# Performance work log

Hardware: AMD Instinct MI355X
Metric: run time of the kernel (lower is better)

The kernel has to match this reference:

```python
import jax, jax.numpy as jnp
import numpy as np

NEG = -100000.0  # matches torch masked_fill constant

def setup_inputs() -> dict:
    key = jax.random.key(0)
    k1, k2, k3, k4 = jax.random.split(key, 4)
    B, T, D, H, S = 8, 2048, 1024, 8, 128
    features = jax.random.normal(k1, (B, T, D), dtype=jnp.float32)
    begins = jax.random.randint(k2, (B, S), 0, 2016, dtype=jnp.int64)
    widths = jax.random.randint(k3, (B, S), 1, 33, dtype=jnp.int64)
    ends = jnp.minimum(begins + widths, T)
    key_w = jax.random.normal(k4, (H, D), dtype=jnp.float32) / np.sqrt(D)
    key_b = jnp.zeros((H,), dtype=jnp.float32)
    return {"features": features, "begins": begins, "ends": ends,
            "key_w": key_w, "key_b": key_b}


def reference(features, begins, ends, key_w, key_b):
    # features: [B, T, D]; begins/ends: [B, S]
    B, T, D = features.shape
    H = key_w.shape[0]
    S = begins.shape[1]
    pos = jnp.arange(T)  # [T]
    # span mask [B, S, T]
    mask = (begins[..., None] <= pos) & (pos < ends[..., None])
    # key projection: [B, T, H]
    logits = jnp.einsum('btd,hd->bth', features, key_w) + key_b
    # masked softmax over T per (batch, span, head): [B, S, T, H]
    masked = jnp.where(mask[..., None], logits[:, None, :, :], NEG)
    weights = jax.nn.softmax(masked, axis=-2)
    # values = features reshaped to heads: [B, T, H, D//H]
    values = features.reshape(B, T, H, D // H)
    res = jnp.einsum('bthd,bsth->bshd', values, weights)  # [B, S, H, D//H]
    return res.reshape(B, S, D)
```

## Files before the change

### kernel.cpp

```cpp
#include <hip/hip_runtime.h>

#define B_  8
#define T_  2048
#define D_  1024
#define H_  8
#define S_  128

__global__ __launch_bounds__(512) void span_pool_kernel(
    const float* __restrict__ feat,
    const int* __restrict__ begins,
    const int* __restrict__ ends,
    const float* __restrict__ kw,
    const float* __restrict__ kb,
    float* __restrict__ out)
{
    const int bs   = blockIdx.x;
    const int b    = bs >> 7;
    const int wv   = threadIdx.x >> 6;
    const int lane = threadIdx.x & 63;

    __shared__ __align__(16) float kwl[H_ * D_];
    __shared__ __align__(16) float wts[32 * H_];

    {
        const float4* src = (const float4*)kw;
        float4*       dst = (float4*)kwl;
        dst[threadIdx.x]        = src[threadIdx.x];
        dst[threadIdx.x + 512]  = src[threadIdx.x + 512];
        dst[threadIdx.x + 1024] = src[threadIdx.x + 1024];
        dst[threadIdx.x + 1536] = src[threadIdx.x + 1536];
    }

    const int begin = begins[bs];
    const int width = ends[bs] - begin;
    const size_t row0 = (size_t)b * T_ + begin;
    const float kbv = (lane < H_) ? kb[lane] : 0.f;

    float4 fv0, fv1, fv2, fv3;
    const int r0 = wv;
    if (r0 < width) {
        const float* fr = feat + (row0 + r0) * D_ + lane * 4;
        fv0 = *(const float4*)(fr +   0);
        fv1 = *(const float4*)(fr + 256);
        fv2 = *(const float4*)(fr + 512);
        fv3 = *(const float4*)(fr + 768);
    }
    __syncthreads();

    for (int r = r0; r < width; r += 8) {
        if (r != r0) {
            const float* fr = feat + (row0 + r) * D_ + lane * 4;
            fv0 = *(const float4*)(fr +   0);
            fv1 = *(const float4*)(fr + 256);
            fv2 = *(const float4*)(fr + 512);
            fv3 = *(const float4*)(fr + 768);
        }
        float acc[H_];
#pragma unroll
        for (int h = 0; h < H_; ++h) {
            const float* kh = &kwl[h * D_ + lane * 4];
            float4 k0 = *(const float4*)(kh +   0);
            float4 k1 = *(const float4*)(kh + 256);
            float4 k2 = *(const float4*)(kh + 512);
            float4 k3 = *(const float4*)(kh + 768);
            acc[h] = fv0.x * k0.x + fv0.y * k0.y + fv0.z * k0.z + fv0.w * k0.w
                   + fv1.x * k1.x + fv1.y * k1.y + fv1.z * k1.z + fv1.w * k1.w
                   + fv2.x * k2.x + fv2.y * k2.y + fv2.z * k2.z + fv2.w * k2.w
                   + fv3.x * k3.x + fv3.y * k3.y + fv3.z * k3.z + fv3.w * k3.w;
        }
#pragma unroll
        for (int s = 0; s < 3; ++s) {
            const int m = 1 << s;
            const bool hi = (lane >> s) & 1;
#pragma unroll
            for (int j = 0; j < (4 >> s); ++j) {
                float mine  = hi ? acc[2 * j + 1] : acc[2 * j];
                float other = hi ? acc[2 * j]     : acc[2 * j + 1];
                acc[j] = mine + __shfl_xor(other, m, 64);
            }
        }
        acc[0] += __shfl_xor(acc[0],  8, 64);
        acc[0] += __shfl_xor(acc[0], 16, 64);
        acc[0] += __shfl_xor(acc[0], 32, 64);

        if (lane < H_)
            wts[r * H_ + lane] = acc[0] + kbv;
    }
    __syncthreads();

    if (threadIdx.x < 64) {
        float4 lv = *(const float4*)&wts[lane * 4];
        const int w8 = width * H_;
        float v0 = (4 * lane + 0 < w8) ? lv.x : -1e30f;
        float v1 = (4 * lane + 1 < w8) ? lv.y : -1e30f;
        float v2 = (4 * lane + 2 < w8) ? lv.z : -1e30f;
        float v3 = (4 * lane + 3 < w8) ? lv.w : -1e30f;

        float m0 = v0, m1 = v1, m2 = v2, m3 = v3;
#pragma unroll
        for (int off = 2; off <= 32; off <<= 1) {
            m0 = fmaxf(m0, __shfl_xor(m0, off, 64));
            m1 = fmaxf(m1, __shfl_xor(m1, off, 64));
            m2 = fmaxf(m2, __shfl_xor(m2, off, 64));
            m3 = fmaxf(m3, __shfl_xor(m3, off, 64));
        }
        float e0 = __expf(v0 - m0);
        float e1 = __expf(v1 - m1);
        float e2 = __expf(v2 - m2);
        float e3 = __expf(v3 - m3);
        float s0 = e0, s1 = e1, s2 = e2, s3 = e3;
#pragma unroll
        for (int off = 2; off <= 32; off <<= 1) {
            s0 += __shfl_xor(s0, off, 64);
            s1 += __shfl_xor(s1, off, 64);
            s2 += __shfl_xor(s2, off, 64);
            s3 += __shfl_xor(s3, off, 64);
        }
        *(float4*)&wts[lane * 4] =
            make_float4(e0 / s0, e1 / s1, e2 / s2, e3 / s3);
    }
    __syncthreads();

    const int c  = threadIdx.x;
    const int h0 = c >> 7;
    const float* fb = feat + row0 * D_;
    float a0 = 0.f, a1 = 0.f;
    for (int k = 0; k < width; ++k) {
        const float* frw = fb + (size_t)k * D_;
        const float w0 = wts[k * H_ + h0];
        const float w1 = wts[k * H_ + h0 + 4];
        a0 += w0 * frw[c];
        a1 += w1 * frw[c + 512];
    }
    out[(size_t)bs * D_ + c]       = a0;
    out[(size_t)bs * D_ + c + 512] = a1;
}

extern "C" void kernel_launch(void* const* d_in, const int* in_sizes, int n_in,
                              void* d_out, int out_size, void* d_ws, size_t ws_size,
                              hipStream_t stream) {
    const float* feat   = (const float*)d_in[0];
    const int*   begins = (const int*)d_in[1];
    const int*   ends   = (const int*)d_in[2];
    const float* kw     = (const float*)d_in[3];
    const float* kb     = (const float*)d_in[4];
    float*       out    = (float*)d_out;
    (void)d_ws; (void)ws_size;

    span_pool_kernel<<<B_ * S_, 512, 0, stream>>>(feat, begins, ends, kw, kb, out);
}
```

Measured before the change: 115.4 us.

## Fuse span softmax and pooling via online softmax with persistent atomic scheduler

Replaces the three-phase per-span kernel (logits to shared memory, softmax, second pass over features) with a single pass in which each wave keeps online-softmax running max, sum and weighted feature accumulators in registers. Per-wave partials are merged across waves through shared memory, so feature rows are read once instead of twice. Blocks become persistent (512 blocks) and pull spans from a global atomic counter reset by an extra tiny kernel launch, with launch bounds raised to allow more resident blocks. This costs an extra launch, per-row exponentials and a larger shared-memory footprint that may limit occupancy.

```diff
diff --git a/kernel.cpp b/kernel.cpp
--- a/kernel.cpp
+++ b/kernel.cpp
@@ -5,22 +5,29 @@
 #define D_  1024
 #define H_  8
 #define S_  128
+#define NSPAN (B_ * S_)
 
-__global__ __launch_bounds__(512) void span_pool_kernel(
+
+__global__ void init_counter(unsigned int* __restrict__ c) { *c = 0u; }
+
+__global__ __launch_bounds__(512, 4) void span_pool_online(
     const float* __restrict__ feat,
     const int* __restrict__ begins,
     const int* __restrict__ ends,
     const float* __restrict__ kw,
     const float* __restrict__ kb,
-    float* __restrict__ out)
+    float* __restrict__ out,
+    unsigned int* __restrict__ counter)
 {
-    const int bs   = blockIdx.x;
-    const int b    = bs >> 7;
     const int wv   = threadIdx.x >> 6;
     const int lane = threadIdx.x & 63;
+    const int hi   = lane >> 5;
 
     __shared__ __align__(16) float kwl[H_ * D_];
-    __shared__ __align__(16) float wts[32 * H_];
+    __shared__ __align__(16) float slab[8 * D_];
+    __shared__ float msm[8 * H_];
+    __shared__ float mss[8 * H_];
+    __shared__ unsigned int s_span;
 
     {
         const float4* src = (const float4*)kw;
@@ -31,109 +38,125 @@
         dst[threadIdx.x + 1536] = src[threadIdx.x + 1536];
     }
 
-    const int begin = begins[bs];
-    const int width = ends[bs] - begin;
-    const size_t row0 = (size_t)b * T_ + begin;
-    const float kbv = (lane < H_) ? kb[lane] : 0.f;
+    const float kbv = kb[lane & 7];
 
-    float4 fv0, fv1, fv2, fv3;
-    const int r0 = wv;
-    if (r0 < width) {
-        const float* fr = feat + (row0 + r0) * D_ + lane * 4;
-        fv0 = *(const float4*)(fr +   0);
-        fv1 = *(const float4*)(fr + 256);
-        fv2 = *(const float4*)(fr + 512);
-        fv3 = *(const float4*)(fr + 768);
+    for (;;) {
+        if (threadIdx.x == 0) s_span = atomicAdd(counter, 1u);
+        __syncthreads();
+        const int s = (int)s_span;
+        if (s >= NSPAN) break;
+
+        const int begin = begins[s];
+        const int width = ends[s] - begin;
+        const size_t row0 = (size_t)(s >> 7) * T_ + begin;
+
+        float4 a0 = make_float4(0.f,0.f,0.f,0.f);
+        float4 a1 = make_float4(0.f,0.f,0.f,0.f);
+        float4 a2 = make_float4(0.f,0.f,0.f,0.f);
+        float4 a3 = make_float4(0.f,0.f,0.f,0.f);
+        float m0=-INFINITY, m1=-INFINITY, m2=-INFINITY, m3=-INFINITY;
+        float sm0=0.f, sm1=0.f, sm2=0.f, sm3=0.f;
+
+        for (int r = wv; r < width; r += 8) {
+            const float* fr = feat + (row0 + r) * D_ + lane * 4;
+            float4 fv0 = *(const float4*)(fr +   0);
+            float4 fv1 = *(const float4*)(fr + 256);
+            float4 fv2 = *(const float4*)(fr + 512);
+            float4 fv3 = *(const float4*)(fr + 768);
+
+            float acc[H_];
+#pragma unroll
+            for (int h = 0; h < H_; ++h) {
+                const float* kh = &kwl[h * D_ + lane * 4];
+                float4 k0 = *(const float4*)(kh +   0);
+                float4 k1 = *(const float4*)(kh + 256);
+                float4 k2 = *(const float4*)(kh + 512);
+                float4 k3 = *(const float4*)(kh + 768);
+                acc[h] = fv0.x*k0.x + fv0.y*k0.y + fv0.z*k0.z + fv0.w*k0.w
+                       + fv1.x*k1.x + fv1.y*k1.y + fv1.z*k1.z + fv1.w*k1.w
+                       + fv2.x*k2.x + fv2.y*k2.y + fv2.z*k2.z + fv2.w*k2.w
+                       + fv3.x*k3.x + fv3.y*k3.y + fv3.z*k3.z + fv3.w*k3.w;
+            }
+#pragma unroll
+            for (int st = 0; st < 3; ++st) {
+                const int mm = 1 << st;
+                const bool hb = (lane >> st) & 1;
+#pragma unroll
+                for (int j = 0; j < (4 >> st); ++j) {
+                    float mine  = hb ? acc[2*j + 1] : acc[2*j];
+                    float other = hb ? acc[2*j]     : acc[2*j + 1];
+                    acc[j] = mine + __shfl_xor(other, mm, 64);
+                }
+            }
+            acc[0] += __shfl_xor(acc[0],  8, 64);
+            acc[0] += __shfl_xor(acc[0], 16, 64);
+            acc[0] += __shfl_xor(acc[0], 32, 64);
+            const float logit = acc[0] + kbv;
+
+            {   const float lj = __shfl(logit, 0 + hi, 64);
+                const float mn = fmaxf(m0, lj);
+                const float c = __expf(m0 - mn), e = __expf(lj - mn);
+                sm0 = sm0*c + e;
+                a0.x = a0.x*c + e*fv0.x; a0.y = a0.y*c + e*fv0.y;
+                a0.z = a0.z*c + e*fv0.z; a0.w = a0.w*c + e*fv0.w;
+                m0 = mn; }
+            {   const float lj = __shfl(logit, 2 + hi, 64);
+                const float mn = fmaxf(m1, lj);
+                const float c = __expf(m1 - mn), e = __expf(lj - mn);
+                sm1 = sm1*c + e;
+                a1.x = a1.x*c + e*fv1.x; a1.y = a1.y*c + e*fv1.y;
+                a1.z = a1.z*c + e*fv1.z; a1.w = a1.w*c + e*fv1.w;
+                m1 = mn; }
+            {   const float lj = __shfl(logit, 4 + hi, 64);
+                const float mn = fmaxf(m2, lj);
+                const float c = __expf(m2 - mn), e = __expf(lj - mn);
+                sm2 = sm2*c + e;
+                a2.x = a2.x*c + e*fv2.x; a2.y = a2.y*c + e*fv2.y;
+                a2.z = a2.z*c + e*fv2.z; a2.w = a2.w*c + e*fv2.w;
+                m2 = mn; }
+            {   const float lj = __shfl(logit, 6 + hi, 64);
+                const float mn = fmaxf(m3, lj);
+                const float c = __expf(m3 - mn), e = __expf(lj - mn);
+                sm3 = sm3*c + e;
+                a3.x = a3.x*c + e*fv3.x; a3.y = a3.y*c + e*fv3.y;
+                a3.z = a3.z*c + e*fv3.z; a3.w = a3.w*c + e*fv3.w;
+                m3 = mn; }
+        }
+
+        *(float4*)&slab[wv*D_ +   0 + lane*4] = a0;
+        *(float4*)&slab[wv*D_ + 256 + lane*4] = a1;
+        *(float4*)&slab[wv*D_ + 512 + lane*4] = a2;
+        *(float4*)&slab[wv*D_ + 768 + lane*4] = a3;
+        if ((lane & 31) == 0) {
+            msm[wv*8 + 0 + hi] = m0;  mss[wv*8 + 0 + hi] = sm0;
+            msm[wv*8 + 2 + hi] = m1;  mss[wv*8 + 2 + hi] = sm1;
+            msm[wv*8 + 4 + hi] = m2;  mss[wv*8 + 4 + hi] = sm2;
+            msm[wv*8 + 6 + hi] = m3;  mss[wv*8 + 6 + hi] = sm3;
+        }
+        __syncthreads();
+
+        const int t  = threadIdx.x;
+        const int ha = t >> 7;
+        const int hb = ha + 4;
+        float Ma = -INFINITY, Mb = -INFINITY;
+#pragma unroll
+        for (int w = 0; w < 8; ++w) {
+            Ma = fmaxf(Ma, msm[w*8 + ha]);
+            Mb = fmaxf(Mb, msm[w*8 + hb]);
+        }
+        float Sa = 0.f, Sb = 0.f, oa = 0.f, ob = 0.f;
+#pragma unroll
+        for (int w = 0; w < 8; ++w) {
+            const float ga = __expf(msm[w*8 + ha] - Ma);
+            const float gb = __expf(msm[w*8 + hb] - Mb);
+            Sa += mss[w*8 + ha] * ga;
+            Sb += mss[w*8 + hb] * gb;
+            oa += slab[w*D_ + t      ] * ga;
+            ob += slab[w*D_ + t + 512] * gb;
+        }
+        out[(size_t)s * D_ + t      ] = oa / Sa;
+        out[(size_t)s * D_ + t + 512] = ob / Sb;
     }
-    __syncthreads();
-
-    for (int r = r0; r < width; r += 8) {
-        if (r != r0) {
-            const float* fr = feat + (row0 + r) * D_ + lane * 4;
-            fv0 = *(const float4*)(fr +   0);
-            fv1 = *(const float4*)(fr + 256);
-            fv2 = *(const float4*)(fr + 512);
-            fv3 = *(const float4*)(fr + 768);
-        }
-        float acc[H_];
-#pragma unroll
-        for (int h = 0; h < H_; ++h) {
-            const float* kh = &kwl[h * D_ + lane * 4];
-            float4 k0 = *(const float4*)(kh +   0);
-            float4 k1 = *(const float4*)(kh + 256);
-            float4 k2 = *(const float4*)(kh + 512);
-            float4 k3 = *(const float4*)(kh + 768);
-            acc[h] = fv0.x * k0.x + fv0.y * k0.y + fv0.z * k0.z + fv0.w * k0.w
-                   + fv1.x * k1.x + fv1.y * k1.y + fv1.z * k1.z + fv1.w * k1.w
-                   + fv2.x * k2.x + fv2.y * k2.y + fv2.z * k2.z + fv2.w * k2.w
-                   + fv3.x * k3.x + fv3.y * k3.y + fv3.z * k3.z + fv3.w * k3.w;
-        }
-#pragma unroll
-        for (int s = 0; s < 3; ++s) {
-            const int m = 1 << s;
-            const bool hi = (lane >> s) & 1;
-#pragma unroll
-            for (int j = 0; j < (4 >> s); ++j) {
-                float mine  = hi ? acc[2 * j + 1] : acc[2 * j];
-                float other = hi ? acc[2 * j]     : acc[2 * j + 1];
-                acc[j] = mine + __shfl_xor(other, m, 64);
-            }
-        }
-        acc[0] += __shfl_xor(acc[0],  8, 64);
-        acc[0] += __shfl_xor(acc[0], 16, 64);
-        acc[0] += __shfl_xor(acc[0], 32, 64);
-
-        if (lane < H_)
-            wts[r * H_ + lane] = acc[0] + kbv;
-    }
-    __syncthreads();
-
-    if (threadIdx.x < 64) {
-        float4 lv = *(const float4*)&wts[lane * 4];
-        const int w8 = width * H_;
-        float v0 = (4 * lane + 0 < w8) ? lv.x : -1e30f;
-        float v1 = (4 * lane + 1 < w8) ? lv.y : -1e30f;
-        float v2 = (4 * lane + 2 < w8) ? lv.z : -1e30f;
-        float v3 = (4 * lane + 3 < w8) ? lv.w : -1e30f;
-
-        float m0 = v0, m1 = v1, m2 = v2, m3 = v3;
-#pragma unroll
-        for (int off = 2; off <= 32; off <<= 1) {
-            m0 = fmaxf(m0, __shfl_xor(m0, off, 64));
-            m1 = fmaxf(m1, __shfl_xor(m1, off, 64));
-            m2 = fmaxf(m2, __shfl_xor(m2, off, 64));
-            m3 = fmaxf(m3, __shfl_xor(m3, off, 64));
-        }
-        float e0 = __expf(v0 - m0);
-        float e1 = __expf(v1 - m1);
-        float e2 = __expf(v2 - m2);
-        float e3 = __expf(v3 - m3);
-        float s0 = e0, s1 = e1, s2 = e2, s3 = e3;
-#pragma unroll
-        for (int off = 2; off <= 32; off <<= 1) {
-            s0 += __shfl_xor(s0, off, 64);
-            s1 += __shfl_xor(s1, off, 64);
-            s2 += __shfl_xor(s2, off, 64);
-            s3 += __shfl_xor(s3, off, 64);
-        }
-        *(float4*)&wts[lane * 4] =
-            make_float4(e0 / s0, e1 / s1, e2 / s2, e3 / s3);
-    }
-    __syncthreads();
-
-    const int c  = threadIdx.x;
-    const int h0 = c >> 7;
-    const float* fb = feat + row0 * D_;
-    float a0 = 0.f, a1 = 0.f;
-    for (int k = 0; k < width; ++k) {
-        const float* frw = fb + (size_t)k * D_;
-        const float w0 = wts[k * H_ + h0];
-        const float w1 = wts[k * H_ + h0 + 4];
-        a0 += w0 * frw[c];
-        a1 += w1 * frw[c + 512];
-    }
-    out[(size_t)bs * D_ + c]       = a0;
-    out[(size_t)bs * D_ + c + 512] = a1;
 }
 
 extern "C" void kernel_launch(void* const* d_in, const int* in_sizes, int n_in,
@@ -145,7 +168,8 @@
     const float* kw     = (const float*)d_in[3];
     const float* kb     = (const float*)d_in[4];
     float*       out    = (float*)d_out;
-    (void)d_ws; (void)ws_size;
+    unsigned int* counter = (unsigned int*)d_ws;
 
-    span_pool_kernel<<<B_ * S_, 512, 0, stream>>>(feat, begins, ends, kw, kb, out);
+    init_counter<<<1, 1, 0, stream>>>(counter);
+    span_pool_online<<<512, 512, 0, stream>>>(feat, begins, ends, kw, kb, out, counter);
 }
```

After: 209.0 us. +81.1%, slower.

## Convert span pooling to a persistent kernel fed by an atomic work queue

Applied to the files above, without the earlier changes.

Launches a fixed grid of 512 persistent blocks. Each block pulls span indices from a global atomic counter and loops until all spans are done, replacing the previous one-block-per-span launch. The aim is to load the key-weight table into shared memory once per block rather than once per span, and to balance uneven span widths dynamically. The cost is an extra tiny kernel launch to reset the counter, one atomic plus a barrier per span, and less latency hiding because the first feature-row prefetch is no longer overlapped with the weight-table load.

```diff
diff --git a/kernel.cpp b/kernel.cpp
--- a/kernel.cpp
+++ b/kernel.cpp
@@ -5,22 +5,27 @@
 #define D_  1024
 #define H_  8
 #define S_  128
+#define NSPAN (B_ * S_)
+#define NBLK  512
 
-__global__ __launch_bounds__(512) void span_pool_kernel(
+
+__global__ void init_counter(unsigned int* __restrict__ c) { *c = 0u; }
+
+__global__ __launch_bounds__(512) void span_pool_v3(
     const float* __restrict__ feat,
     const int* __restrict__ begins,
     const int* __restrict__ ends,
     const float* __restrict__ kw,
     const float* __restrict__ kb,
-    float* __restrict__ out)
+    float* __restrict__ out,
+    unsigned int* __restrict__ counter)
 {
-    const int bs   = blockIdx.x;
-    const int b    = bs >> 7;
     const int wv   = threadIdx.x >> 6;
     const int lane = threadIdx.x & 63;
 
     __shared__ __align__(16) float kwl[H_ * D_];
     __shared__ __align__(16) float wts[32 * H_];
+    __shared__ unsigned int s_span;
 
     {
         const float4* src = (const float4*)kw;
@@ -31,109 +36,103 @@
         dst[threadIdx.x + 1536] = src[threadIdx.x + 1536];
     }
 
-    const int begin = begins[bs];
-    const int width = ends[bs] - begin;
-    const size_t row0 = (size_t)b * T_ + begin;
     const float kbv = (lane < H_) ? kb[lane] : 0.f;
 
-    float4 fv0, fv1, fv2, fv3;
-    const int r0 = wv;
-    if (r0 < width) {
-        const float* fr = feat + (row0 + r0) * D_ + lane * 4;
-        fv0 = *(const float4*)(fr +   0);
-        fv1 = *(const float4*)(fr + 256);
-        fv2 = *(const float4*)(fr + 512);
-        fv3 = *(const float4*)(fr + 768);
+    for (;;) {
+        if (threadIdx.x == 0) s_span = atomicAdd(counter, 1u);
+        __syncthreads();
+        const int s = (int)s_span;
+        if (s >= NSPAN) break;
+
+        const int begin = begins[s];
+        const int width = ends[s] - begin;
+        const size_t row0 = (size_t)(s >> 7) * T_ + begin;
+
+        for (int r = wv; r < width; r += 8) {
+            const float* fr = feat + (row0 + r) * D_ + lane * 4;
+            float4 fv0 = *(const float4*)(fr +   0);
+            float4 fv1 = *(const float4*)(fr + 256);
+            float4 fv2 = *(const float4*)(fr + 512);
+            float4 fv3 = *(const float4*)(fr + 768);
+
+            float acc[H_];
+#pragma unroll
+            for (int h = 0; h < H_; ++h) {
+                const float* kh = &kwl[h * D_ + lane * 4];
+                float4 k0 = *(const float4*)(kh +   0);
+                float4 k1 = *(const float4*)(kh + 256);
+                float4 k2 = *(const float4*)(kh + 512);
+                float4 k3 = *(const float4*)(kh + 768);
+                acc[h] = fv0.x*k0.x + fv0.y*k0.y + fv0.z*k0.z + fv0.w*k0.w
+                       + fv1.x*k1.x + fv1.y*k1.y + fv1.z*k1.z + fv1.w*k1.w
+                       + fv2.x*k2.x + fv2.y*k2.y + fv2.z*k2.z + fv2.w*k2.w
+                       + fv3.x*k3.x + fv3.y*k3.y + fv3.z*k3.z + fv3.w*k3.w;
+            }
+#pragma unroll
+            for (int st = 0; st < 3; ++st) {
+                const int mm = 1 << st;
+                const bool hb = (lane >> st) & 1;
+#pragma unroll
+                for (int j = 0; j < (4 >> st); ++j) {
+                    float mine  = hb ? acc[2*j + 1] : acc[2*j];
+                    float other = hb ? acc[2*j]     : acc[2*j + 1];
+                    acc[j] = mine + __shfl_xor(other, mm, 64);
+                }
+            }
+            acc[0] += __shfl_xor(acc[0],  8, 64);
+            acc[0] += __shfl_xor(acc[0], 16, 64);
+            acc[0] += __shfl_xor(acc[0], 32, 64);
+
+            if (lane < H_)
+                wts[r * H_ + lane] = acc[0] + kbv;
+        }
+        __syncthreads();
+
+        if (threadIdx.x < 64) {
+            float4 lv = *(const float4*)&wts[lane * 4];
+            const int w8 = width * H_;
+            float v0 = (4 * lane + 0 < w8) ? lv.x : -1e30f;
+            float v1 = (4 * lane + 1 < w8) ? lv.y : -1e30f;
+            float v2 = (4 * lane + 2 < w8) ? lv.z : -1e30f;
+            float v3 = (4 * lane + 3 < w8) ? lv.w : -1e30f;
+
+            float m0 = v0, m1 = v1, m2 = v2, m3 = v3;
+#pragma unroll
+            for (int off = 2; off <= 32; off <<= 1) {
+                m0 = fmaxf(m0, __shfl_xor(m0, off, 64));
+                m1 = fmaxf(m1, __shfl_xor(m1, off, 64));
+                m2 = fmaxf(m2, __shfl_xor(m2, off, 64));
+                m3 = fmaxf(m3, __shfl_xor(m3, off, 64));
+            }
+            float e0 = __expf(v0 - m0);
+            float e1 = __expf(v1 - m1);
+            float e2 = __expf(v2 - m2);
+            float e3 = __expf(v3 - m3);
+            float s0 = e0, s1 = e1, s2 = e2, s3 = e3;
+#pragma unroll
+            for (int off = 2; off <= 32; off <<= 1) {
+                s0 += __shfl_xor(s0, off, 64);
+                s1 += __shfl_xor(s1, off, 64);
+                s2 += __shfl_xor(s2, off, 64);
+                s3 += __shfl_xor(s3, off, 64);
+            }
+            *(float4*)&wts[lane * 4] =
+                make_float4(e0 / s0, e1 / s1, e2 / s2, e3 / s3);
+        }
+        __syncthreads();
+
+        const int t  = threadIdx.x;
+        const int ha = t >> 7;
+        const float* fb = feat + row0 * D_;
+        float a0 = 0.f, a1 = 0.f;
+        for (int k = 0; k < width; ++k) {
+            const float* frw = fb + (size_t)k * D_;
+            a0 += wts[k * H_ + ha]     * frw[t];
+            a1 += wts[k * H_ + ha + 4] * frw[t + 512];
+        }
+        out[(size_t)s * D_ + t]       = a0;
+        out[(size_t)s * D_ + t + 512] = a1;
     }
-    __syncthreads();
-
-    for (int r = r0; r < width; r += 8) {
-        if (r != r0) {
-            const float* fr = feat + (row0 + r) * D_ + lane * 4;
-            fv0 = *(const float4*)(fr +   0);
-            fv1 = *(const float4*)(fr + 256);
-            fv2 = *(const float4*)(fr + 512);
-            fv3 = *(const float4*)(fr + 768);
-        }
-        float acc[H_];
-#pragma unroll
-        for (int h = 0; h < H_; ++h) {
-            const float* kh = &kwl[h * D_ + lane * 4];
-            float4 k0 = *(const float4*)(kh +   0);
-            float4 k1 = *(const float4*)(kh + 256);
-            float4 k2 = *(const float4*)(kh + 512);
-            float4 k3 = *(const float4*)(kh + 768);
-            acc[h] = fv0.x * k0.x + fv0.y * k0.y + fv0.z * k0.z + fv0.w * k0.w
-                   + fv1.x * k1.x + fv1.y * k1.y + fv1.z * k1.z + fv1.w * k1.w
-                   + fv2.x * k2.x + fv2.y * k2.y + fv2.z * k2.z + fv2.w * k2.w
-                   + fv3.x * k3.x + fv3.y * k3.y + fv3.z * k3.z + fv3.w * k3.w;
-        }
-#pragma unroll
-        for (int s = 0; s < 3; ++s) {
-            const int m = 1 << s;
-            const bool hi = (lane >> s) & 1;
-#pragma unroll
-            for (int j = 0; j < (4 >> s); ++j) {
-                float mine  = hi ? acc[2 * j + 1] : acc[2 * j];
-                float other = hi ? acc[2 * j]     : acc[2 * j + 1];
-                acc[j] = mine + __shfl_xor(other, m, 64);
-            }
-        }
-        acc[0] += __shfl_xor(acc[0],  8, 64);
-        acc[0] += __shfl_xor(acc[0], 16, 64);
-        acc[0] += __shfl_xor(acc[0], 32, 64);
-
-        if (lane < H_)
-            wts[r * H_ + lane] = acc[0] + kbv;
-    }
-    __syncthreads();
-
-    if (threadIdx.x < 64) {
-        float4 lv = *(const float4*)&wts[lane * 4];
-        const int w8 = width * H_;
-        float v0 = (4 * lane + 0 < w8) ? lv.x : -1e30f;
-        float v1 = (4 * lane + 1 < w8) ? lv.y : -1e30f;
-        float v2 = (4 * lane + 2 < w8) ? lv.z : -1e30f;
-        float v3 = (4 * lane + 3 < w8) ? lv.w : -1e30f;
-
-        float m0 = v0, m1 = v1, m2 = v2, m3 = v3;
-#pragma unroll
-        for (int off = 2; off <= 32; off <<= 1) {
-            m0 = fmaxf(m0, __shfl_xor(m0, off, 64));
-            m1 = fmaxf(m1, __shfl_xor(m1, off, 64));
-            m2 = fmaxf(m2, __shfl_xor(m2, off, 64));
-            m3 = fmaxf(m3, __shfl_xor(m3, off, 64));
-        }
-        float e0 = __expf(v0 - m0);
-        float e1 = __expf(v1 - m1);
-        float e2 = __expf(v2 - m2);
-        float e3 = __expf(v3 - m3);
-        float s0 = e0, s1 = e1, s2 = e2, s3 = e3;
-#pragma unroll
-        for (int off = 2; off <= 32; off <<= 1) {
-            s0 += __shfl_xor(s0, off, 64);
-            s1 += __shfl_xor(s1, off, 64);
-            s2 += __shfl_xor(s2, off, 64);
-            s3 += __shfl_xor(s3, off, 64);
-        }
-        *(float4*)&wts[lane * 4] =
-            make_float4(e0 / s0, e1 / s1, e2 / s2, e3 / s3);
-    }
-    __syncthreads();
-
-    const int c  = threadIdx.x;
-    const int h0 = c >> 7;
-    const float* fb = feat + row0 * D_;
-    float a0 = 0.f, a1 = 0.f;
-    for (int k = 0; k < width; ++k) {
-        const float* frw = fb + (size_t)k * D_;
-        const float w0 = wts[k * H_ + h0];
-        const float w1 = wts[k * H_ + h0 + 4];
-        a0 += w0 * frw[c];
-        a1 += w1 * frw[c + 512];
-    }
-    out[(size_t)bs * D_ + c]       = a0;
-    out[(size_t)bs * D_ + c + 512] = a1;
 }
 
 extern "C" void kernel_launch(void* const* d_in, const int* in_sizes, int n_in,
@@ -145,7 +144,8 @@
     const float* kw     = (const float*)d_in[3];
     const float* kb     = (const float*)d_in[4];
     float*       out    = (float*)d_out;
-    (void)d_ws; (void)ws_size;
+    unsigned int* counter = (unsigned int*)d_ws;
 
-    span_pool_kernel<<<B_ * S_, 512, 0, stream>>>(feat, begins, ends, kw, kb, out);
+    init_counter<<<1, 1, 0, stream>>>(counter);
+    span_pool_v3<<<NBLK, 512, 0, stream>>>(feat, begins, ends, kw, kb, out, counter);
 }
```

Result: no change. 116.4 us (+0.9%).
